# Optimization experiments

Measured on AMD Instinct MI355X. Metric: run time of the kernel, lower is better.

## Reference

```python
import jax, jax.numpy as jnp
import numpy as np

NUM_CLASSES = 80
STRIDES = (8, 16, 32)
RADIUS = 2.5
BOX_WEIGHT = 5.0
BIG = 1e9  # emulates restriction of cost/matching to union-candidate anchors
CAND_K = 10


def setup_inputs() -> dict:
    key = jax.random.key(0)
    ks = jax.random.split(key, 6)
    B, G = 16, 16
    p0 = jax.random.normal(ks[0], (B, NUM_CLASSES + 5, 160, 160), jnp.float32)
    p1 = jax.random.normal(ks[1], (B, NUM_CLASSES + 5, 80, 80), jnp.float32)
    p2 = jax.random.normal(ks[2], (B, NUM_CLASSES + 5, 40, 40), jnp.float32)
    cxy = jax.random.uniform(ks[3], (B, G, 2), jnp.float32, 64.0, 1216.0)
    wh = jax.random.uniform(ks[4], (B, G, 2), jnp.float32, 16.0, 256.0)
    cls = jax.random.randint(ks[5], (B, G, 1), 0, NUM_CLASSES).astype(jnp.float32)
    labels = jnp.concatenate([cxy, wh, cls], axis=-1)  # [B,G,5] xywh + class id
    return {"p0": p0, "p1": p1, "p2": p2, "labels": labels}


def _decode(p, stride):
    # [B,C,H,W] -> [B,HW,C] with xy=(xy+grid)*stride, wh=exp(wh)*stride
    B, C, H, W = p.shape
    out = jnp.transpose(p.reshape(B, C, H * W), (0, 2, 1))
    yy, xx = jnp.meshgrid(jnp.arange(H, dtype=p.dtype), jnp.arange(W, dtype=p.dtype), indexing='ij')
    gx, gy = xx.reshape(-1), yy.reshape(-1)
    xy = (out[..., :2] + jnp.stack([gx, gy], axis=-1)) * stride
    wh = jnp.exp(out[..., 2:4]) * stride
    return jnp.concatenate([xy, wh, out[..., 4:]], axis=-1), gx, gy


def _pair_iou(a, b):
    # a:[G,4], b:[A,4] in xywh -> [G,A]
    a1, a2 = a[:, :2] - a[:, 2:] * 0.5, a[:, :2] + a[:, 2:] * 0.5
    b1, b2 = b[:, :2] - b[:, 2:] * 0.5, b[:, :2] + b[:, 2:] * 0.5
    tl = jnp.maximum(a1[:, None], b1[None])
    br = jnp.minimum(a2[:, None], b2[None])
    wh = jnp.maximum(br - tl, 0.0)
    inter = wh[..., 0] * wh[..., 1]
    return inter / (a[:, 2] * a[:, 3])[:, None].__add__((b[:, 2] * b[:, 3])[None]).__sub__(inter).__add__(1e-16)


def _elem_iou(a, b):
    # elementwise xywh iou on [...,4]
    a1, a2 = a[..., :2] - a[..., 2:] * 0.5, a[..., :2] + a[..., 2:] * 0.5
    b1, b2 = b[..., :2] - b[..., 2:] * 0.5, b[..., :2] + b[..., 2:] * 0.5
    wh = jnp.maximum(jnp.minimum(a2, b2) - jnp.maximum(a1, b1), 0.0)
    inter = wh[..., 0] * wh[..., 1]
    return inter / (a[..., 2] * a[..., 3] + b[..., 2] * b[..., 3] - inter + 1e-16)


def _bce_logits(x, t):
    return jnp.maximum(x, 0.0) - x * t + jnp.log1p(jnp.exp(-jnp.abs(x)))


def _assign(tb, tc, pbox, pcls_l, pconf_l, xc, yc, sv):
    # Per-image SimOTA. tb:[G,4] tc:[G] pbox:[A,4] pcls_l:[A,C] pconf_l:[A]
    G = tb.shape[0]
    bx, by, bw, bh = tb[:, 0:1], tb[:, 1:2], tb[:, 2:3], tb[:, 3:4]
    in_box = (xc[None] > bx - bw * 0.5) & (xc[None] < bx + bw * 0.5) & \
             (yc[None] > by - bh * 0.5) & (yc[None] < by + bh * 0.5)  # [G,A]
    r = RADIUS * sv[None]
    in_mir = (xc[None] > bx - r) & (xc[None] < bx + r) & (yc[None] > by - r) & (yc[None] < by + r)
    union = jnp.any(in_box, 0) | jnp.any(in_mir, 0)  # [A]
    inter = in_box & in_mir  # [G,A]
    iou = _pair_iou(tb, pbox)  # [G,A]
    # cls cost: BCE(sqrt(sigmoid(cls)*sigmoid(conf)), one_hot) summed over classes
    p = jnp.sqrt(jax.nn.sigmoid(pcls_l) * jax.nn.sigmoid(pconf_l)[:, None])  # [A,C]
    logp = jnp.clip(jnp.log(p), -100.0, None)
    log1mp = jnp.clip(jnp.log1p(-p), -100.0, None)
    base = -log1mp.sum(-1)  # [A] = sum_c -log(1-p)
    cls_cost = base[None] - logp[:, tc].T + log1mp[:, tc].T  # [G,A]
    cost = cls_cost - 3.0 * jnp.log(iou + 1e-8) + 1e5 * (~inter) + BIG * (~union)[None]
    iou_m = jnp.where(union[None], iou, 0.0)
    dyn_k = jnp.maximum(jax.lax.top_k(iou_m, CAND_K)[0].sum(1).astype(jnp.int32), 1)  # [G]
    _, idx = jax.lax.top_k(-cost, CAND_K)  # per-gt lowest-cost anchors, sorted
    sel = (jnp.arange(CAND_K)[None] < dyn_k[:, None]).astype(cost.dtype)  # [G,K]
    matching = jnp.zeros_like(cost).at[jnp.arange(G)[:, None], idx].max(sel)  # [G,A]
    conflict = matching.sum(0) > 1.0
    gt_min = jnp.argmin(cost, axis=0)  # [A]
    onehot_min = (jnp.arange(G)[:, None] == gt_min[None]).astype(cost.dtype)
    matching = jnp.where(conflict[None], onehot_min, matching)
    fg = matching.sum(0) > 0.0  # [A]
    gidx = jnp.argmax(matching, axis=0)  # [A]
    miou = (matching * iou).sum(0)  # [A]
    t_cls = jax.nn.one_hot(tc[gidx], NUM_CLASSES, dtype=cost.dtype) * miou[:, None]  # [A,C]
    t_box = tb[gidx]  # [A,4]
    return fg, t_cls, t_box


def _forward(p0, p1, p2, labels):
    outs, xcs, ycs, svs = [], [], [], []
    for p, s in zip((p0, p1, p2), STRIDES):
        o, gx, gy = _decode(p, float(s))
        outs.append(o)
        xcs.append((gx + 0.5) * s)
        ycs.append((gy + 0.5) * s)
        svs.append(jnp.full_like(gx, s))
    out = jnp.concatenate(outs, axis=1)  # [B,A,85]
    xc, yc, sv = jnp.concatenate(xcs), jnp.concatenate(ycs), jnp.concatenate(svs)
    pbox, pconf, pcls = out[..., :4], out[..., 4], out[..., 5:]
    tb, tc = labels[..., :4], labels[..., 4].astype(jnp.int32)
    assign = jax.vmap(_assign, in_axes=(0, 0, 0, 0, 0, None, None, None))
    fg, t_cls, t_box = jax.lax.stop_gradient(assign(tb, tc, pbox, pcls, pconf, xc, yc, sv))
    fgf = fg.astype(pbox.dtype)  # target_conf == final fg mask
    loss_box = (fgf * (1.0 - _elem_iou(pbox, t_box) ** 2)).sum()
    loss_conf = _bce_logits(pconf, fgf).sum()
    loss_cls = (fgf[..., None] * _bce_logits(pcls, t_cls)).sum()
    fg_num = jnp.maximum(fgf.sum(), 1.0)
    return (BOX_WEIGHT * loss_box + loss_conf + loss_cls) / fg_num


def reference(p0, p1, p2, labels):
    return _forward(p0, p1, p2, labels)
```

## Files before the change

kernel.cpp:

```cpp
#include <hip/hip_runtime.h>
#include <hip/hip_bf16.h>
#include <cstdint>

#define NCLS 80
#define GNUM 16
#define BNUM 16
#define A0   25600
#define A1   6400
#define A2   1600
#define ATOT 33600
#define NBLK_A 132
#define NBLK_TOTAL (NBLK_A*BNUM)
#define NSPLIT 8
#define SEG   4200
#define WSEG  1050
#define NWAVE 32
#define FINF  3.4e38f
#define IINF  0x7fffffff

__device__ __forceinline__ float rcpf(float x){ return __builtin_amdgcn_rcpf(x); }
__device__ __forceinline__ float sqf (float x){ return __builtin_amdgcn_sqrtf(x); }
__device__ __forceinline__ float rsqf(float x){ return __builtin_amdgcn_rsqf(x); }

__device__ __forceinline__ float bce(float x, float t){
  float e = __expf(-fabsf(x));
  return fmaxf(x,0.f) - x*t + __logf(1.f + e);
}

__device__ __forceinline__ void get_level(const float* p0, const float* p1, const float* p2,
                                          int a, const float*& p, int& hw, int& off, int& W, float& s)
{
  if (a < A0){ p=p0; hw=A0; off=a; W=160; s=8.f; }
  else if (a < A0+A1){ p=p1; hw=A1; off=a-A0; W=80; s=16.f; }
  else { p=p2; hw=A2; off=a-A0-A1; W=40; s=32.f; }
}

__global__ __launch_bounds__(256) void decode_cost_kernel(
    const float* __restrict__ p0, const float* __restrict__ p1, const float* __restrict__ p2,
    const float* __restrict__ labels,
    float* __restrict__ cost, float4* __restrict__ pbox, float* __restrict__ pconf,
    unsigned char* __restrict__ unionm)
{
  const int b = blockIdx.y;
  const int a = blockIdx.x*256 + threadIdx.x;
  __shared__ float s_tb[GNUM][4];
  __shared__ int   s_tc[GNUM];
  if (threadIdx.x < GNUM){
    const float* L = labels + ((size_t)b*GNUM + threadIdx.x)*5;
    s_tb[threadIdx.x][0]=L[0]; s_tb[threadIdx.x][1]=L[1];
    s_tb[threadIdx.x][2]=L[2]; s_tb[threadIdx.x][3]=L[3];
    s_tc[threadIdx.x]=(int)L[4];
  }
  __syncthreads();
  if (a >= ATOT) return;

  const float* p; int hw, off, W; float s;
  get_level(p0,p1,p2,a,p,hw,off,W,s);
  const float* bp = p + (size_t)b*(NCLS+5)*hw + off;

  float rx = bp[0];
  float ry = bp[(size_t)hw];
  float rw = bp[2*(size_t)hw];
  float rh = bp[3*(size_t)hw];
  float cl = bp[4*(size_t)hw];
  int gx = off % W, gy = off / W;
  float px=(rx+gx)*s, py=(ry+gy)*s, pw=__expf(rw)*s, ph=__expf(rh)*s;
  float xc=(gx+0.5f)*s, yc=(gy+0.5f)*s;
  float sc = rcpf(1.f + __expf(-cl));

  float basec = 0.f;
  for (int c=0;c<NCLS;c++){
    float x  = bp[(size_t)(5+c)*hw];
    float u  = sc * rcpf(1.f + __expf(-x));
    float pm = sqf(u);
    float l1 = __logf(1.f - pm);
    basec   -= fmaxf(l1, -100.f);
  }
  float cdiff_g[GNUM];
  #pragma unroll
  for (int g=0;g<GNUM;g++){
    float x  = bp[(size_t)(5+s_tc[g])*hw];
    float u  = sc * rcpf(1.f + __expf(-x));
    float rp = rsqf(u);
    cdiff_g[g] = __logf(fmaxf(rp - 1.f, 1e-30f));
  }

  float p1x=px-pw*0.5f, p2x=px+pw*0.5f, p1y=py-ph*0.5f, p2y=py+ph*0.5f;
  float areaP = pw*ph;
  float r = 2.5f*s;
  bool unionf=false;
  float costs[GNUM];
  #pragma unroll
  for (int g=0;g<GNUM;g++){
    float bx=s_tb[g][0], by=s_tb[g][1], bw=s_tb[g][2], bh=s_tb[g][3];
    float b1x=bx-bw*0.5f, b2x=bx+bw*0.5f, b1y=by-bh*0.5f, b2y=by+bh*0.5f;
    bool inb = (xc>b1x)&&(xc<b2x)&&(yc>b1y)&&(yc<b2y);
    bool inm = (xc>bx-r)&&(xc<bx+r)&&(yc>by-r)&&(yc<by+r);
    unionf = unionf || inb || inm;
    bool inter = inb && inm;
    float tlx=fmaxf(b1x,p1x), brx=fminf(b2x,p2x);
    float tly=fmaxf(b1y,p1y), bry=fminf(b2y,p2y);
    float iw=fmaxf(brx-tlx,0.f), ih=fmaxf(bry-tly,0.f);
    float inte=iw*ih;
    float iou = inte * rcpf(bw*bh+areaP-inte+1e-16f);
    costs[g] = (basec + cdiff_g[g]) - 3.f*__logf(iou+1e-8f) + (inter?0.f:100000.f);
  }
  float add = unionf?0.f:1e9f;
  size_t rowbase = (size_t)b*GNUM*ATOT + a;
  #pragma unroll
  for (int g=0;g<GNUM;g++) cost[rowbase + (size_t)g*ATOT] = costs[g]+add;
  pbox [(size_t)b*ATOT+a] = make_float4(px,py,pw,ph);
  pconf[(size_t)b*ATOT+a] = cl;
  unionm[(size_t)b*ATOT+a] = unionf?1:0;
}

__global__ __launch_bounds__(256) void topk_stage1(
    const float* __restrict__ cost, const float4* __restrict__ pbox,
    const unsigned char* __restrict__ unionm, const float* __restrict__ labels,
    float* __restrict__ cand_c, int* __restrict__ cand_i, float* __restrict__ cand_v)
{
  const int bg   = blockIdx.y;
  const int b    = bg >> 4;
  const int seg  = blockIdx.x;
  const int wave = threadIdx.x >> 6;
  const int lane = threadIdx.x & 63;
  const int wg   = seg*4 + wave;

  const float*  crow = cost + (size_t)bg*ATOT;
  const float4* prow = pbox + (size_t)b*ATOT;
  const unsigned char* urow = unionm + (size_t)b*ATOT;
  const float bx = labels[bg*5+0], by = labels[bg*5+1];
  const float bw = labels[bg*5+2], bh = labels[bg*5+3];
  const float areaB = bw*bh;
  const float b1x=bx-bw*0.5f, b2x=bx+bw*0.5f, b1y=by-bh*0.5f, b2y=by+bh*0.5f;

  const int start = seg*SEG + wave*WSEG;
  const int end   = start + WSEG;

  float cv[10]; int ci[10]; float iv[10];
  #pragma unroll
  for (int k=0;k<10;k++){ cv[k]=FINF; ci[k]=IINF; iv[k]=0.f; }

  for (int a = start + lane; a < end; a += 64){
    float c = crow[a];
    if (c < cv[9] || (c == cv[9] && a < ci[9])){
      float nc=c; int ni=a;
      #pragma unroll
      for (int k=0;k<10;k++){
        bool better = (nc < cv[k]) || (nc==cv[k] && ni<ci[k]);
        float tv=cv[k]; int ti=ci[k];
        cv[k]=better?nc:cv[k]; ci[k]=better?ni:ci[k];
        nc  =better?tv:nc;     ni  =better?ti:ni;
      }
    }
    if (urow[a]){
      float4 pb = prow[a];
      float tlx=fmaxf(b1x, pb.x-pb.z*0.5f), brx=fminf(b2x, pb.x+pb.z*0.5f);
      float tly=fmaxf(b1y, pb.y-pb.w*0.5f), bry=fminf(b2y, pb.y+pb.w*0.5f);
      float iw=fmaxf(brx-tlx,0.f), ih=fmaxf(bry-tly,0.f);
      float inte=iw*ih;
      float io = inte * rcpf(areaB + pb.z*pb.w - inte + 1e-16f);
      if (io > iv[9]){
        float nv=io;
        #pragma unroll
        for (int k=0;k<10;k++){
          bool better = nv > iv[k];
          float tv=iv[k];
          iv[k]=better?nv:iv[k];
          nv  =better?tv:nv;
        }
      }
    }
  }

  float selc = 0.f; int seli = 0;
  #pragma unroll
  for (int r=0;r<10;r++){
    float bv = cv[0]; int bi = ci[0];
    #pragma unroll
    for (int off=32; off>0; off>>=1){
      float ov = __shfl_xor(bv, off);
      int   oi = __shfl_xor(bi, off);
      bool take = (ov < bv) || (ov==bv && oi<bi);
      bv = take?ov:bv; bi = take?oi:bi;
    }
    if (lane == r){ selc = bv; seli = bi; }
    if (cv[0]==bv && ci[0]==bi){
      #pragma unroll
      for (int k=0;k<9;k++){ cv[k]=cv[k+1]; ci[k]=ci[k+1]; }
      cv[9]=FINF; ci[9]=IINF;
    }
  }
  float selv = 0.f;
  #pragma unroll
  for (int r=0;r<10;r++){
    float bv = iv[0]; int bl = lane;
    #pragma unroll
    for (int off=32; off>0; off>>=1){
      float ov = __shfl_xor(bv, off);
      int   ol = __shfl_xor(bl, off);
      bool take = (ov > bv) || (ov==bv && ol<bl);
      bv = take?ov:bv; bl = take?ol:bl;
    }
    if (lane == r) selv = bv;
    if (lane == bl){
      #pragma unroll
      for (int k=0;k<9;k++){ iv[k]=iv[k+1]; }
      iv[9]=0.f;
    }
  }

  if (lane < 10){
    const size_t base = ((size_t)bg*NWAVE + wg)*10 + lane;
    cand_c[base] = selc;
    cand_i[base] = seli;
    cand_v[base] = selv;
  }
}

__global__ __launch_bounds__(64) void topk_stage2(
    const float* __restrict__ cand_c, const int* __restrict__ cand_i,
    const float* __restrict__ cand_v, unsigned int* __restrict__ match_mask)
{
  const int bg = blockIdx.x;
  const int b = bg >> 4, g = bg & 15;
  const int lane = threadIdx.x;
  const size_t base = (size_t)bg*NWAVE*10 + lane*5;

  float cv[5]; int ci[5]; float iv[5];
  #pragma unroll
  for (int k=0;k<5;k++){ cv[k]=cand_c[base+k]; ci[k]=cand_i[base+k]; iv[k]=cand_v[base+k]; }

  int seli = 0;
  #pragma unroll
  for (int r=0;r<10;r++){
    float bv = cv[0]; int bi = ci[0];
    #pragma unroll
    for (int off=32; off>0; off>>=1){
      float ov = __shfl_xor(bv, off);
      int   oi = __shfl_xor(bi, off);
      bool take = (ov < bv) || (ov==bv && oi<bi);
      bv = take?ov:bv; bi = take?oi:bi;
    }
    if (lane == r) seli = bi;
    if (cv[0]==bv && ci[0]==bi){
      #pragma unroll
      for (int k=0;k<4;k++){ cv[k]=cv[k+1]; ci[k]=ci[k+1]; }
      cv[4]=FINF; ci[4]=IINF;
    }
  }

  float isum = 0.f;
  #pragma unroll
  for (int r=0;r<10;r++){
    float bv = iv[0]; int bl = lane;
    #pragma unroll
    for (int off=32; off>0; off>>=1){
      float ov = __shfl_xor(bv, off);
      int   ol = __shfl_xor(bl, off);
      bool take = (ov > bv) || (ov==bv && ol<bl);
      bv = take?ov:bv; bl = take?ol:bl;
    }
    isum += bv;
    if (lane == bl){
      #pragma unroll
      for (int k=0;k<4;k++){ iv[k]=iv[k+1]; }
      iv[4]=0.f;
    }
  }

  int dynk = (int)isum;
  if (dynk < 1)  dynk = 1;
  if (dynk > 10) dynk = 10;
  if (lane < dynk)
    atomicOr(&match_mask[(size_t)b*ATOT + seli], 1u<<g);
}

__global__ __launch_bounds__(256) void loss_kernel(
    const float* __restrict__ p0, const float* __restrict__ p1, const float* __restrict__ p2,
    const float* __restrict__ labels,
    const float* __restrict__ cost, const float4* __restrict__ pbox,
    const float* __restrict__ pconf, const unsigned int* __restrict__ match_mask,
    float* __restrict__ blocksums)
{
  const int b = blockIdx.y;
  const int a = blockIdx.x*256 + threadIdx.x;
  float lbox=0.f, lconf=0.f, lcls=0.f, fgn=0.f;
  if (a < ATOT){
    unsigned int m = match_mask[(size_t)b*ATOT+a];
    float cl = pconf[(size_t)b*ATOT+a];
    if (m != 0u){
      int gidx;
      if (__popc(m) > 1){
        float best = FINF; int bgi = 0;
        for (int g=0; g<GNUM; g++){
          float c = cost[((size_t)b*GNUM+g)*ATOT + a];
          if (c < best){ best=c; bgi=g; }
        }
        gidx = bgi;
      } else {
        gidx = __ffs(m)-1;
      }
      const float* L = labels + ((size_t)b*GNUM+gidx)*5;
      float bx=L[0], by=L[1], bw=L[2], bh=L[3];
      int tcg=(int)L[4];
      float4 pb = pbox[(size_t)b*ATOT+a];
      float tlx=fmaxf(bx-bw*0.5f, pb.x-pb.z*0.5f);
      float brx=fminf(bx+bw*0.5f, pb.x+pb.z*0.5f);
      float tly=fmaxf(by-bh*0.5f, pb.y-pb.w*0.5f);
      float bry=fminf(by+bh*0.5f, pb.y+pb.w*0.5f);
      float iw=fmaxf(brx-tlx,0.f), ih=fmaxf(bry-tly,0.f);
      float inte=iw*ih;
      float iou = inte * rcpf(bw*bh + pb.z*pb.w - inte + 1e-16f);
      lbox = 1.f - iou*iou;
      lconf = bce(cl, 1.f);
      float miou = iou;
      const float* p; int hw, off, W; float s;
      get_level(p0,p1,p2,a,p,hw,off,W,s);
      const float* bp = p + (size_t)b*(NCLS+5)*hw + off;
      for (int c=0;c<NCLS;c++){
        float x = bp[(size_t)(5+c)*hw];
        float t = (c==tcg)? miou : 0.f;
        lcls += bce(x, t);
      }
      fgn = 1.f;
    } else {
      lconf = bce(cl, 0.f);
    }
  }
  #pragma unroll
  for (int off2=32; off2>0; off2>>=1){
    lbox  += __shfl_down(lbox,  off2);
    lconf += __shfl_down(lconf, off2);
    lcls  += __shfl_down(lcls,  off2);
    fgn   += __shfl_down(fgn,   off2);
  }
  __shared__ float s_red[4][4];
  const int wave = threadIdx.x >> 6;
  if ((threadIdx.x & 63)==0){
    s_red[wave][0]=lbox; s_red[wave][1]=lconf; s_red[wave][2]=lcls; s_red[wave][3]=fgn;
  }
  __syncthreads();
  if (threadIdx.x==0){
    float r0=0,r1=0,r2=0,r3=0;
    #pragma unroll
    for (int w=0;w<4;w++){ r0+=s_red[w][0]; r1+=s_red[w][1]; r2+=s_red[w][2]; r3+=s_red[w][3]; }
    const int bid = blockIdx.y*gridDim.x + blockIdx.x;
    ((float4*)blocksums)[bid] = make_float4(r0,r1,r2,r3);
  }
}

__global__ __launch_bounds__(256) void finalize_kernel(
    const float* __restrict__ blocksums, float* __restrict__ out)
{
  const int tid = threadIdx.x;
  float r0=0,r1=0,r2=0,r3=0;
  for (int i = tid; i < NBLK_TOTAL; i += 256){
    const float4 v = ((const float4*)blocksums)[i];
    r0+=v.x; r1+=v.y; r2+=v.z; r3+=v.w;
  }
  #pragma unroll
  for (int off=32; off>0; off>>=1){
    r0 += __shfl_down(r0, off);
    r1 += __shfl_down(r1, off);
    r2 += __shfl_down(r2, off);
    r3 += __shfl_down(r3, off);
  }
  __shared__ float s_red[4][4];
  const int wave = tid >> 6;
  if ((tid & 63)==0){ s_red[wave][0]=r0; s_red[wave][1]=r1; s_red[wave][2]=r2; s_red[wave][3]=r3; }
  __syncthreads();
  if (tid==0){
    float t0=0,t1=0,t2=0,t3=0;
    #pragma unroll
    for (int w=0;w<4;w++){ t0+=s_red[w][0]; t1+=s_red[w][1]; t2+=s_red[w][2]; t3+=s_red[w][3]; }
    out[0] = (5.f*t0 + t1 + t2) / fmaxf(t3, 1.f);
  }
}

extern "C" void kernel_launch(void* const* d_in, const int* in_sizes, int n_in,
                              void* d_out, int out_size, void* d_ws, size_t ws_size,
                              hipStream_t stream)
{
  const float* p0     = (const float*)d_in[0];
  const float* p1     = (const float*)d_in[1];
  const float* p2     = (const float*)d_in[2];
  const float* labels = (const float*)d_in[3];

  char* ws = (char*)d_ws;
  size_t o = 0;
  float*        cost       = (float*)(ws + o);        o += (size_t)BNUM*GNUM*ATOT*4;
  float4*       pbox       = (float4*)(ws + o);       o += (size_t)BNUM*ATOT*16;
  float*        pconf      = (float*)(ws + o);        o += (size_t)BNUM*ATOT*4;
  unsigned int* match_mask = (unsigned int*)(ws + o); o += (size_t)BNUM*ATOT*4;
  unsigned char* unionm    = (unsigned char*)(ws + o);o += (size_t)BNUM*ATOT;
  o = (o + 255) & ~(size_t)255;
  float*        blocksums  = (float*)(ws + o);        o += (size_t)NBLK_TOTAL*4*4;
  o = (o + 255) & ~(size_t)255;
  float*        cand_c     = (float*)(ws + o);        o += (size_t)256*NWAVE*10*4;
  int*          cand_i     = (int*)(ws + o);          o += (size_t)256*NWAVE*10*4;
  float*        cand_v     = (float*)(ws + o);        o += (size_t)256*NWAVE*10*4;

  hipMemsetAsync(match_mask, 0, (size_t)BNUM*ATOT*4, stream);

  dim3 gridA((ATOT+255)/256, BNUM);
  decode_cost_kernel<<<gridA, 256, 0, stream>>>(p0,p1,p2,labels,cost,pbox,pconf,unionm);
  dim3 gridT(NSPLIT, BNUM*GNUM);
  topk_stage1<<<gridT, 256, 0, stream>>>(cost, pbox, unionm, labels, cand_c, cand_i, cand_v);
  topk_stage2<<<BNUM*GNUM, 64, 0, stream>>>(cand_c, cand_i, cand_v, match_mask);
  loss_kernel<<<gridA, 256, 0, stream>>>(p0,p1,p2,labels,cost,pbox,pconf,match_mask,blocksums);
  finalize_kernel<<<1, 256, 0, stream>>>(blocksums, (float*)d_out);
}
```

Before: 145.1 us.

## Process two anchors per thread and batch class log terms into products

The decode/cost kernel now handles two adjacent anchors per thread with float2 loads and stores, halving its grid. The per-class base cost replaces 80 separate logs with products of eight terms followed by one log per group, using sqrt(sc)*rsqrt(1+e) in place of sqrt(sc*sigmoid). The intent is to cut transcendental-instruction count and widen memory transactions. The product form may lose precision or underflow, and the new loss-kernel grid constant is kept equal to the old anchor-block count.

```diff
diff --git a/kernel.cpp b/kernel.cpp
--- a/kernel.cpp
+++ b/kernel.cpp
@@ -9,6 +9,7 @@
 #define A1   6400
 #define A2   1600
 #define ATOT 33600
+#define QTOT 16800
 #define NBLK_A 132
 #define NBLK_TOTAL (NBLK_A*BNUM)
 #define NSPLIT 8
@@ -42,7 +43,7 @@
     unsigned char* __restrict__ unionm)
 {
   const int b = blockIdx.y;
-  const int a = blockIdx.x*256 + threadIdx.x;
+  const int q = blockIdx.x*256 + threadIdx.x;
   __shared__ float s_tb[GNUM][4];
   __shared__ int   s_tc[GNUM];
   if (threadIdx.x < GNUM){
@@ -52,66 +53,103 @@
     s_tc[threadIdx.x]=(int)L[4];
   }
   __syncthreads();
-  if (a >= ATOT) return;
+  if (q >= QTOT) return;
+  const int a0 = q*2;
 
   const float* p; int hw, off, W; float s;
-  get_level(p0,p1,p2,a,p,hw,off,W,s);
+  get_level(p0,p1,p2,a0,p,hw,off,W,s);
   const float* bp = p + (size_t)b*(NCLS+5)*hw + off;
 
-  float rx = bp[0];
-  float ry = bp[(size_t)hw];
-  float rw = bp[2*(size_t)hw];
-  float rh = bp[3*(size_t)hw];
-  float cl = bp[4*(size_t)hw];
-  int gx = off % W, gy = off / W;
-  float px=(rx+gx)*s, py=(ry+gy)*s, pw=__expf(rw)*s, ph=__expf(rh)*s;
-  float xc=(gx+0.5f)*s, yc=(gy+0.5f)*s;
-  float sc = rcpf(1.f + __expf(-cl));
-
-  float basec = 0.f;
-  for (int c=0;c<NCLS;c++){
-    float x  = bp[(size_t)(5+c)*hw];
-    float u  = sc * rcpf(1.f + __expf(-x));
-    float pm = sqf(u);
-    float l1 = __logf(1.f - pm);
-    basec   -= fmaxf(l1, -100.f);
-  }
-  float cdiff_g[GNUM];
+  const float2 RX = *(const float2*)(bp);
+  const float2 RY = *(const float2*)(bp + (size_t)hw);
+  const float2 RW = *(const float2*)(bp + 2*(size_t)hw);
+  const float2 RH = *(const float2*)(bp + 3*(size_t)hw);
+  const float2 CL = *(const float2*)(bp + 4*(size_t)hw);
+
+  int gx0 = off % W, gy0 = off / W;
+  int gx1 = gx0+1, gy1 = gy0; if (gx1 >= W){ gx1 = 0; gy1++; }
+
+  const float sc0 = rcpf(1.f + __expf(-CL.x));
+  const float sc1 = rcpf(1.f + __expf(-CL.y));
+  const float ssc0 = sqf(sc0),   ssc1 = sqf(sc1);
+  const float rssc0 = rcpf(ssc0), rssc1 = rcpf(ssc1);
+
+  const float* cp = bp + 5*(size_t)hw;
+  float base0=0.f, base1=0.f;
+  #pragma unroll 1
+  for (int grp=0; grp<10; grp++){
+    float pr0=1.f, pr1=1.f;
+    #pragma unroll
+    for (int j=0;j<8;j++){
+      const float2 x = *(const float2*)(cp + (size_t)(grp*8+j)*hw);
+      float e0 = __expf(-x.x), e1 = __expf(-x.y);
+      pr0 *= (1.f - ssc0*rsqf(1.f+e0));
+      pr1 *= (1.f - ssc1*rsqf(1.f+e1));
+    }
+    base0 -= __logf(pr0);
+    base1 -= __logf(pr1);
+  }
+
+  const float px0=(RX.x+gx0)*s, py0=(RY.x+gy0)*s, pw0=__expf(RW.x)*s, ph0=__expf(RH.x)*s;
+  const float px1=(RX.y+gx1)*s, py1=(RY.y+gy1)*s, pw1=__expf(RW.y)*s, ph1=__expf(RH.y)*s;
+  const float xc0=(gx0+0.5f)*s, yc0=(gy0+0.5f)*s;
+  const float xc1=(gx1+0.5f)*s, yc1=(gy1+0.5f)*s;
+  const float q1x0=px0-pw0*0.5f, q2x0=px0+pw0*0.5f, q1y0=py0-ph0*0.5f, q2y0=py0+ph0*0.5f;
+  const float q1x1=px1-pw1*0.5f, q2x1=px1+pw1*0.5f, q1y1=py1-ph1*0.5f, q2y1=py1+ph1*0.5f;
+  const float areaP0 = pw0*ph0, areaP1 = pw1*ph1;
+  const float r = 2.5f*s;
+
+  bool un0=false, un1=false;
   #pragma unroll
   for (int g=0;g<GNUM;g++){
-    float x  = bp[(size_t)(5+s_tc[g])*hw];
-    float u  = sc * rcpf(1.f + __expf(-x));
-    float rp = rsqf(u);
-    cdiff_g[g] = __logf(fmaxf(rp - 1.f, 1e-30f));
-  }
-
-  float p1x=px-pw*0.5f, p2x=px+pw*0.5f, p1y=py-ph*0.5f, p2y=py+ph*0.5f;
-  float areaP = pw*ph;
-  float r = 2.5f*s;
-  bool unionf=false;
-  float costs[GNUM];
-  #pragma unroll
+    const float bx=s_tb[g][0], by=s_tb[g][1], bw=s_tb[g][2], bh=s_tb[g][3];
+    const float b1x=bx-bw*0.5f, b2x=bx+bw*0.5f, b1y=by-bh*0.5f, b2y=by+bh*0.5f;
+    un0 = un0 || ((xc0>b1x)&&(xc0<b2x)&&(yc0>b1y)&&(yc0<b2y))
+              || ((xc0>bx-r)&&(xc0<bx+r)&&(yc0>by-r)&&(yc0<by+r));
+    un1 = un1 || ((xc1>b1x)&&(xc1<b2x)&&(yc1>b1y)&&(yc1<b2y))
+              || ((xc1>bx-r)&&(xc1<bx+r)&&(yc1>by-r)&&(yc1<by+r));
+  }
+  const float add0 = un0?0.f:1e9f, add1 = un1?0.f:1e9f;
+
+  const size_t rowb = (size_t)b*GNUM*ATOT + a0;
+  #pragma unroll 1
   for (int g=0;g<GNUM;g++){
-    float bx=s_tb[g][0], by=s_tb[g][1], bw=s_tb[g][2], bh=s_tb[g][3];
-    float b1x=bx-bw*0.5f, b2x=bx+bw*0.5f, b1y=by-bh*0.5f, b2y=by+bh*0.5f;
-    bool inb = (xc>b1x)&&(xc<b2x)&&(yc>b1y)&&(yc<b2y);
-    bool inm = (xc>bx-r)&&(xc<bx+r)&&(yc>by-r)&&(yc<by+r);
-    unionf = unionf || inb || inm;
-    bool inter = inb && inm;
-    float tlx=fmaxf(b1x,p1x), brx=fminf(b2x,p2x);
-    float tly=fmaxf(b1y,p1y), bry=fminf(b2y,p2y);
-    float iw=fmaxf(brx-tlx,0.f), ih=fmaxf(bry-tly,0.f);
-    float inte=iw*ih;
-    float iou = inte * rcpf(bw*bh+areaP-inte+1e-16f);
-    costs[g] = (basec + cdiff_g[g]) - 3.f*__logf(iou+1e-8f) + (inter?0.f:100000.f);
-  }
-  float add = unionf?0.f:1e9f;
-  size_t rowbase = (size_t)b*GNUM*ATOT + a;
-  #pragma unroll
-  for (int g=0;g<GNUM;g++) cost[rowbase + (size_t)g*ATOT] = costs[g]+add;
-  pbox [(size_t)b*ATOT+a] = make_float4(px,py,pw,ph);
-  pconf[(size_t)b*ATOT+a] = cl;
-  unionm[(size_t)b*ATOT+a] = unionf?1:0;
+    const float2 x = *(const float2*)(cp + (size_t)s_tc[g]*hw);
+    const float e0 = __expf(-x.x), e1 = __expf(-x.y);
+    const float rp0 = rssc0*sqf(1.f+e0), rp1 = rssc1*sqf(1.f+e1);
+    const float cd0 = __logf(fmaxf(rp0-1.f, 1e-30f));
+    const float cd1 = __logf(fmaxf(rp1-1.f, 1e-30f));
+
+    const float bx=s_tb[g][0], by=s_tb[g][1], bw=s_tb[g][2], bh=s_tb[g][3];
+    const float b1x=bx-bw*0.5f, b2x=bx+bw*0.5f, b1y=by-bh*0.5f, b2y=by+bh*0.5f;
+    const float areaB = bw*bh;
+
+    const bool inb0 = (xc0>b1x)&&(xc0<b2x)&&(yc0>b1y)&&(yc0<b2y);
+    const bool inm0 = (xc0>bx-r)&&(xc0<bx+r)&&(yc0>by-r)&&(yc0<by+r);
+    const bool inb1 = (xc1>b1x)&&(xc1<b2x)&&(yc1>b1y)&&(yc1<b2y);
+    const bool inm1 = (xc1>bx-r)&&(xc1<bx+r)&&(yc1>by-r)&&(yc1<by+r);
+
+    float iw,ih,inte;
+    iw = fmaxf(fminf(b2x,q2x0)-fmaxf(b1x,q1x0),0.f);
+    ih = fmaxf(fminf(b2y,q2y0)-fmaxf(b1y,q1y0),0.f);
+    inte = iw*ih;
+    const float iou0 = inte * rcpf(areaB+areaP0-inte+1e-16f);
+    iw = fmaxf(fminf(b2x,q2x1)-fmaxf(b1x,q1x1),0.f);
+    ih = fmaxf(fminf(b2y,q2y1)-fmaxf(b1y,q1y1),0.f);
+    inte = iw*ih;
+    const float iou1 = inte * rcpf(areaB+areaP1-inte+1e-16f);
+
+    float2 cst;
+    cst.x = base0 + cd0 - 3.f*__logf(iou0+1e-8f) + ((inb0&&inm0)?0.f:100000.f) + add0;
+    cst.y = base1 + cd1 - 3.f*__logf(iou1+1e-8f) + ((inb1&&inm1)?0.f:100000.f) + add1;
+    *(float2*)(cost + rowb + (size_t)g*ATOT) = cst;
+  }
+
+  pbox[(size_t)b*ATOT+a0  ] = make_float4(px0,py0,pw0,ph0);
+  pbox[(size_t)b*ATOT+a0+1] = make_float4(px1,py1,pw1,ph1);
+  *(float2*)(pconf + (size_t)b*ATOT + a0) = make_float2(CL.x, CL.y);
+  uchar2 um; um.x = un0?1:0; um.y = un1?1:0;
+  *(uchar2*)(unionm + (size_t)b*ATOT + a0) = um;
 }
 
 __global__ __launch_bounds__(256) void topk_stage1(
@@ -403,11 +441,12 @@
 
   hipMemsetAsync(match_mask, 0, (size_t)BNUM*ATOT*4, stream);
 
-  dim3 gridA((ATOT+255)/256, BNUM);
+  dim3 gridA((QTOT+255)/256, BNUM);
   decode_cost_kernel<<<gridA, 256, 0, stream>>>(p0,p1,p2,labels,cost,pbox,pconf,unionm);
   dim3 gridT(NSPLIT, BNUM*GNUM);
   topk_stage1<<<gridT, 256, 0, stream>>>(cost, pbox, unionm, labels, cand_c, cand_i, cand_v);
   topk_stage2<<<BNUM*GNUM, 64, 0, stream>>>(cand_c, cand_i, cand_v, match_mask);
-  loss_kernel<<<gridA, 256, 0, stream>>>(p0,p1,p2,labels,cost,pbox,pconf,match_mask,blocksums);
+  dim3 gridC(NBLK_A, BNUM);
+  loss_kernel<<<gridC, 256, 0, stream>>>(p0,p1,p2,labels,cost,pbox,pconf,match_mask,blocksums);
   finalize_kernel<<<1, 256, 0, stream>>>(blocksums, (float*)d_out);
 }
```

Result: faster. 140.6 us (-3.1%).
